# Kernel tuning notes

Measured on AMD Instinct MI355X. Metric: run time of the kernel, lower is better.

## Reference

```python
import jax, jax.numpy as jnp
import numpy as np

TEMPERATURE = 1.0  # forward default
INIT_STD = 0.01    # per-class gate init: N(0, 0.01)

def setup_inputs() -> dict:
    key = jax.random.key(0)
    kf, kws, kw1, kw2 = jax.random.split(key, 4)
    B, F, H, C, E = 256, 2048, 512, 512, 8
    Hh = H // 2  # 256
    features = jax.random.normal(kf, (B, F), dtype=jnp.float32)
    # shared transform Linear(F, H) -- default torch init approximated by small normal
    Ws = jax.random.normal(kws, (F, H), dtype=jnp.float32) * (1.0 / np.sqrt(F))
    bs = jnp.zeros((H,), dtype=jnp.float32)
    # per-class gates, stacked over class dim: N(0, 0.01) init, zero bias (as in module)
    W1 = jax.random.normal(kw1, (C, H, Hh), dtype=jnp.float32) * INIT_STD
    b1 = jnp.zeros((C, Hh), dtype=jnp.float32)
    W2 = jax.random.normal(kw2, (C, Hh, E), dtype=jnp.float32) * INIT_STD
    b2 = jnp.zeros((C, E), dtype=jnp.float32)
    return {"features": features, "Ws": Ws, "bs": bs, "W1": W1, "b1": b1, "W2": W2, "b2": b2}

def reference(features, Ws, bs, W1, b1, W2, b2):
    # shared transform: Linear -> ReLU (Dropout is identity at inference)
    shared = jax.nn.relu(features @ Ws + bs)                      # [B, H]
    # batched per-class MLP: one grouped GEMM across all classes
    h = jax.nn.relu(jnp.einsum('bh,chk->bck', shared, W1) + b1)   # [B, C, H/2]
    gate_logits = jnp.einsum('bck,cke->bce', h, W2) + b2          # [B, C, E]
    gate_weights = jax.nn.softmax(gate_logits / TEMPERATURE, axis=-1)
    return (gate_weights, gate_logits)
```

## Files before the change

### kernel.cpp

```cpp
#include <hip/hip_runtime.h>
#include <hip/hip_bf16.h>

#define BATCH 256
#define F_DIM 2048
#define H_DIM 512
#define HH    256
#define NCLS  512
#define E_DIM 8

typedef __attribute__((ext_vector_type(8))) short  bf16x8;
typedef __attribute__((ext_vector_type(4))) float  f32x4;
typedef __attribute__((ext_vector_type(4))) unsigned short u16x4;

__device__ __forceinline__ unsigned short f2bf(float x) {
    union { float f; unsigned int u; } v; v.f = x;
    unsigned int r = v.u + 0x7fffu + ((v.u >> 16) & 1u);
    return (unsigned short)(r >> 16);
}

__global__ __launch_bounds__(256) void k_gemm1(
    const float* __restrict__ features,
    const float* __restrict__ Ws,
    float* __restrict__ partials)
{
    const int tid = threadIdx.x;
    const int lane = tid & 63;
    const int wave = tid >> 6;
    const int job = blockIdx.x * 4 + wave;
    const int kidx = job & 7;
    const int ng  = (job >> 3) & 7;
    const int mt  = job >> 6;
    const int l15 = lane & 15, quad = lane >> 4;
    const int m0 = mt * 16, n0 = ng * 64, kb = kidx * 256;

    f32x4 z = {0.f, 0.f, 0.f, 0.f};
    f32x4 acc[4];
#pragma unroll
    for (int nf = 0; nf < 4; ++nf) acc[nf] = z;

#pragma unroll
    for (int ks = 0; ks < 8; ++ks) {
        const int kk = kb + ks * 32 + quad * 8;
        f32x4 a0 = *(const f32x4*)(features + (size_t)(m0 + l15) * F_DIM + kk);
        f32x4 a1 = *(const f32x4*)(features + (size_t)(m0 + l15) * F_DIM + kk + 4);
        bf16x8 aF;
#pragma unroll
        for (int j = 0; j < 4; ++j) { aF[j] = (short)f2bf(a0[j]); aF[4 + j] = (short)f2bf(a1[j]); }
#pragma unroll
        for (int nf = 0; nf < 4; ++nf) {
            bf16x8 bF;
#pragma unroll
            for (int j = 0; j < 8; ++j)
                bF[j] = (short)f2bf(Ws[(size_t)(kk + j) * H_DIM + n0 + nf * 16 + l15]);
            acc[nf] = __builtin_amdgcn_mfma_f32_16x16x32_bf16(aF, bF, acc[nf], 0, 0, 0);
        }
    }
    float* po = partials + (size_t)kidx * (BATCH * H_DIM);
#pragma unroll
    for (int nf = 0; nf < 4; ++nf)
#pragma unroll
        for (int r = 0; r < 4; ++r)
            po[(size_t)(m0 + quad * 4 + r) * H_DIM + n0 + nf * 16 + l15] = acc[nf][r];
}

__global__ __launch_bounds__(256) void k_reduce_relu(
    const float* __restrict__ partials, const float* __restrict__ bs,
    unsigned short* __restrict__ sharedA)
{
    const int idx = (blockIdx.x * 256 + threadIdx.x) * 4;
    f32x4 s = *(const f32x4*)(partials + idx);
#pragma unroll
    for (int p = 1; p < 8; ++p)
        s += *(const f32x4*)(partials + (size_t)p * (BATCH * H_DIM) + idx);
    s += *(const f32x4*)(bs + (idx & (H_DIM - 1)));
    u16x4 o;
#pragma unroll
    for (int j = 0; j < 4; ++j) {
        float v = s[j] > 0.f ? s[j] : 0.f;
        o[j] = f2bf(v);
    }
    *(u16x4*)(sharedA + idx) = o;
}

__global__ __launch_bounds__(256, 3) void k_main(
    const unsigned short* __restrict__ sharedA,
    const float* __restrict__ W1,
    const float* __restrict__ b1,
    const float* __restrict__ W2,
    float* __restrict__ part4)
{
    const int c = blockIdx.x >> 2;
    const int q = blockIdx.x & 3;
    const int tid = threadIdx.x;
    const int lane = tid & 63;
    const int wave = tid >> 6;
    const int l15 = lane & 15;
    const int quad = lane >> 4;
    const int m0w = wave * 64;
    const int colL = tid & 63;
    const int kseg = tid >> 6;

    const float* __restrict__ W1cq = W1 + (size_t)c * (H_DIM * HH) + q * 64;

    __shared__ unsigned short buf[2][8 * 64 * 8];

    f32x4 z = {0.f, 0.f, 0.f, 0.f};
    f32x4 acc[4][4];
#pragma unroll
    for (int mf = 0; mf < 4; ++mf)
#pragma unroll
        for (int nf = 0; nf < 4; ++nf) acc[mf][nf] = z;

    float rg[16];
#pragma unroll
    for (int j = 0; j < 16; ++j)
        rg[j] = W1cq[(size_t)(kseg * 16 + j) * HH + colL];

#pragma unroll
    for (int ch = 0; ch < 8; ++ch) {
        unsigned short* bp = &buf[ch & 1][0];
#pragma unroll
        for (int h = 0; h < 2; ++h) {
            bf16x8 v;
#pragma unroll
            for (int j = 0; j < 8; ++j) v[j] = (short)f2bf(rg[h * 8 + j]);
            const int kg = kseg * 2 + h;
            *(bf16x8*)(bp + ((kg * 64 + colL) << 3)) = v;
        }
        __syncthreads();
        if (ch < 7) {
#pragma unroll
            for (int j = 0; j < 16; ++j)
                rg[j] = W1cq[(size_t)((ch + 1) * 64 + kseg * 16 + j) * HH + colL];
        }
#pragma unroll
        for (int ks = 0; ks < 2; ++ks) {
            const int k0 = ch * 64 + ks * 32 + quad * 8;
            bf16x8 aF[4];
#pragma unroll
            for (int mf = 0; mf < 4; ++mf)
                aF[mf] = *(const bf16x8*)(sharedA + (size_t)(m0w + mf * 16 + l15) * H_DIM + k0);
#pragma unroll
            for (int nf = 0; nf < 4; ++nf) {
                bf16x8 bF = *(const bf16x8*)(bp + (((ks * 4 + quad) * 64 + nf * 16 + l15) << 3));
#pragma unroll
                for (int mf = 0; mf < 4; ++mf)
                    acc[mf][nf] = __builtin_amdgcn_mfma_f32_16x16x32_bf16(aF[mf], bF, acc[mf][nf], 0, 0, 0);
            }
        }
    }

    const int cq = q * 64;
    float b1v[4];
    f32x4 w2a[4], w2b[4];
#pragma unroll
    for (int nf = 0; nf < 4; ++nf) {
        const int col = cq + nf * 16 + l15;
        b1v[nf] = b1[(size_t)c * HH + col];
        w2a[nf] = *(const f32x4*)(W2 + ((size_t)c * HH + col) * E_DIM);
        w2b[nf] = *(const f32x4*)(W2 + ((size_t)c * HH + col) * E_DIM + 4);
    }

#pragma unroll
    for (int mf = 0; mf < 4; ++mf) {
        float part[4][E_DIM];
#pragma unroll
        for (int r = 0; r < 4; ++r)
#pragma unroll
            for (int e = 0; e < E_DIM; ++e) part[r][e] = 0.f;
#pragma unroll
        for (int nf = 0; nf < 4; ++nf) {
#pragma unroll
            for (int r = 0; r < 4; ++r) {
                float h = acc[mf][nf][r] + b1v[nf];
                h = h > 0.f ? h : 0.f;
                part[r][0] += h * w2a[nf][0]; part[r][1] += h * w2a[nf][1];
                part[r][2] += h * w2a[nf][2]; part[r][3] += h * w2a[nf][3];
                part[r][4] += h * w2b[nf][0]; part[r][5] += h * w2b[nf][1];
                part[r][6] += h * w2b[nf][2]; part[r][7] += h * w2b[nf][3];
            }
        }
#pragma unroll
        for (int r = 0; r < 4; ++r)
#pragma unroll
            for (int e = 0; e < E_DIM; ++e) {
                float v = part[r][e];
                v += __shfl_xor(v, 1, 16);
                v += __shfl_xor(v, 2, 16);
                v += __shfl_xor(v, 4, 16);
                v += __shfl_xor(v, 8, 16);
                part[r][e] = v;
            }
        if (l15 == 0) {
#pragma unroll
            for (int r = 0; r < 4; ++r) {
                const int row = m0w + mf * 16 + quad * 4 + r;
                f32x4 lo = {part[r][0], part[r][1], part[r][2], part[r][3]};
                f32x4 hi = {part[r][4], part[r][5], part[r][6], part[r][7]};
                float* dst = part4 + (((size_t)q * NCLS + c) * BATCH + row) * E_DIM;
                *(f32x4*)dst = lo;
                *(f32x4*)(dst + 4) = hi;
            }
        }
    }
}

__global__ __launch_bounds__(256) void k_softmax(
    const float* __restrict__ part4,
    const float* __restrict__ b2,
    float* __restrict__ out)
{
    const int c = blockIdx.x;
    const int b = threadIdx.x;

    f32x4 lg0 = {0.f, 0.f, 0.f, 0.f}, lg1 = {0.f, 0.f, 0.f, 0.f};
#pragma unroll
    for (int qq = 0; qq < 4; ++qq) {
        const float* p = part4 + (((size_t)qq * NCLS + c) * BATCH + b) * E_DIM;
        lg0 += *(const f32x4*)p;
        lg1 += *(const f32x4*)(p + 4);
    }
    lg0 += *(const f32x4*)(b2 + (size_t)c * E_DIM);
    lg1 += *(const f32x4*)(b2 + (size_t)c * E_DIM + 4);

    float lg[8] = {lg0[0], lg0[1], lg0[2], lg0[3], lg1[0], lg1[1], lg1[2], lg1[3]};
    float mx = lg[0];
#pragma unroll
    for (int e = 1; e < 8; ++e) mx = lg[e] > mx ? lg[e] : mx;
    float ex[8], s = 0.f;
#pragma unroll
    for (int e = 0; e < 8; ++e) { ex[e] = __expf(lg[e] - mx); s += ex[e]; }
    const float inv = 1.f / s;

    const size_t ob = ((size_t)b * NCLS + c) * E_DIM;
    f32x4 w0 = {ex[0] * inv, ex[1] * inv, ex[2] * inv, ex[3] * inv};
    f32x4 w1 = {ex[4] * inv, ex[5] * inv, ex[6] * inv, ex[7] * inv};
    *(f32x4*)(out + ob) = w0;
    *(f32x4*)(out + ob + 4) = w1;
    const size_t lbase = (size_t)BATCH * NCLS * E_DIM;
    f32x4 o0 = {lg[0], lg[1], lg[2], lg[3]};
    f32x4 o1 = {lg[4], lg[5], lg[6], lg[7]};
    *(f32x4*)(out + lbase + ob) = o0;
    *(f32x4*)(out + lbase + ob + 4) = o1;
}

extern "C" void kernel_launch(void* const* d_in, const int* in_sizes, int n_in,
                              void* d_out, int out_size, void* d_ws, size_t ws_size,
                              hipStream_t stream) {
    const float* features = (const float*)d_in[0];
    const float* Ws       = (const float*)d_in[1];
    const float* bs       = (const float*)d_in[2];
    const float* W1       = (const float*)d_in[3];
    const float* b1       = (const float*)d_in[4];
    const float* W2       = (const float*)d_in[5];
    const float* b2       = (const float*)d_in[6];
    float* out = (float*)d_out;

    char* ws = (char*)d_ws;
    float*          parts   = (float*)ws;
    float*          part4   = (float*)ws;
    unsigned short* sharedA = (unsigned short*)(ws + 16777216);

    hipLaunchKernelGGL(k_gemm1,       dim3(256),  dim3(256), 0, stream, features, Ws, parts);
    hipLaunchKernelGGL(k_reduce_relu, dim3(128),  dim3(256), 0, stream, parts, bs, sharedA);
    hipLaunchKernelGGL(k_main,        dim3(2048), dim3(256), 0, stream, sharedA, W1, b1, W2, part4);
    hipLaunchKernelGGL(k_softmax,     dim3(NCLS), dim3(256), 0, stream, part4, b2, out);
}
```

Measured before the change: 454.9 us.

## Load W1 fragments directly into registers, dropping LDS staging and barriers

The main kernel no longer stages W1 through a double-buffered shared-memory tile with __syncthreads. Each wave now loads its own B fragments straight from global memory into registers, two k-steps ahead, converting to bf16 just before the MFMA. The A fragments are prefetched the same way. This removes LDS traffic and barriers, but all four waves now load the same W1 columns redundantly, register pressure goes up (occupancy hint lowered from 3 to 2), and the global loads are narrow scalar strided accesses.

```diff
diff --git a/kernel.cpp b/kernel.cpp
--- a/kernel.cpp
+++ b/kernel.cpp
@@ -82,7 +82,7 @@
     *(u16x4*)(sharedA + idx) = o;
 }
 
-__global__ __launch_bounds__(256, 3) void k_main(
+__global__ __launch_bounds__(256, 2) void k_main(
     const unsigned short* __restrict__ sharedA,
     const float* __restrict__ W1,
     const float* __restrict__ b1,
@@ -97,12 +97,9 @@
     const int l15 = lane & 15;
     const int quad = lane >> 4;
     const int m0w = wave * 64;
-    const int colL = tid & 63;
-    const int kseg = tid >> 6;
-
-    const float* __restrict__ W1cq = W1 + (size_t)c * (H_DIM * HH) + q * 64;
-
-    __shared__ unsigned short buf[2][8 * 64 * 8];
+    const int n0 = q * 64;
+
+    const float* __restrict__ W1cq = W1 + (size_t)c * (H_DIM * HH) + n0;
 
     f32x4 z = {0.f, 0.f, 0.f, 0.f};
     f32x4 acc[4][4];
@@ -111,51 +108,55 @@
 #pragma unroll
         for (int nf = 0; nf < 4; ++nf) acc[mf][nf] = z;
 
-    float rg[16];
-#pragma unroll
-    for (int j = 0; j < 16; ++j)
-        rg[j] = W1cq[(size_t)(kseg * 16 + j) * HH + colL];
-
-#pragma unroll
-    for (int ch = 0; ch < 8; ++ch) {
-        unsigned short* bp = &buf[ch & 1][0];
-#pragma unroll
-        for (int h = 0; h < 2; ++h) {
-            bf16x8 v;
-#pragma unroll
-            for (int j = 0; j < 8; ++j) v[j] = (short)f2bf(rg[h * 8 + j]);
-            const int kg = kseg * 2 + h;
-            *(bf16x8*)(bp + ((kg * 64 + colL) << 3)) = v;
-        }
-        __syncthreads();
-        if (ch < 7) {
-#pragma unroll
-            for (int j = 0; j < 16; ++j)
-                rg[j] = W1cq[(size_t)((ch + 1) * 64 + kseg * 16 + j) * HH + colL];
-        }
-#pragma unroll
-        for (int ks = 0; ks < 2; ++ks) {
-            const int k0 = ch * 64 + ks * 32 + quad * 8;
-            bf16x8 aF[4];
+    float  braw[2][32];
+    bf16x8 aS[2][4];
+
+#pragma unroll
+    for (int s = 0; s < 2; ++s) {
+#pragma unroll
+        for (int nf = 0; nf < 4; ++nf)
+#pragma unroll
+            for (int jj = 0; jj < 8; ++jj)
+                braw[s][nf * 8 + jj] =
+                    W1cq[(size_t)(s * 32 + quad * 8 + jj) * HH + nf * 16 + l15];
+#pragma unroll
+        for (int mf = 0; mf < 4; ++mf)
+            aS[s][mf] = *(const bf16x8*)(sharedA + (size_t)(m0w + mf * 16 + l15) * H_DIM + s * 32 + quad * 8);
+    }
+
+#pragma unroll
+    for (int ks = 0; ks < 16; ++ks) {
+        const int cur = ks & 1;
+        bf16x8 bF[4];
+#pragma unroll
+        for (int nf = 0; nf < 4; ++nf)
+#pragma unroll
+            for (int jj = 0; jj < 8; ++jj)
+                bF[nf][jj] = (short)f2bf(braw[cur][nf * 8 + jj]);
+#pragma unroll
+        for (int nf = 0; nf < 4; ++nf)
 #pragma unroll
             for (int mf = 0; mf < 4; ++mf)
-                aF[mf] = *(const bf16x8*)(sharedA + (size_t)(m0w + mf * 16 + l15) * H_DIM + k0);
-#pragma unroll
-            for (int nf = 0; nf < 4; ++nf) {
-                bf16x8 bF = *(const bf16x8*)(bp + (((ks * 4 + quad) * 64 + nf * 16 + l15) << 3));
-#pragma unroll
-                for (int mf = 0; mf < 4; ++mf)
-                    acc[mf][nf] = __builtin_amdgcn_mfma_f32_16x16x32_bf16(aF[mf], bF, acc[mf][nf], 0, 0, 0);
-            }
-        }
-    }
-
-    const int cq = q * 64;
+                acc[mf][nf] = __builtin_amdgcn_mfma_f32_16x16x32_bf16(aS[cur][mf], bF[nf], acc[mf][nf], 0, 0, 0);
+        if (ks + 2 < 16) {
+            const int kb = (ks + 2) * 32;
+#pragma unroll
+            for (int nf = 0; nf < 4; ++nf)
+#pragma unroll
+                for (int jj = 0; jj < 8; ++jj)
+                    braw[cur][nf * 8 + jj] =
+                        W1cq[(size_t)(kb + quad * 8 + jj) * HH + nf * 16 + l15];
+#pragma unroll
+            for (int mf = 0; mf < 4; ++mf)
+                aS[cur][mf] = *(const bf16x8*)(sharedA + (size_t)(m0w + mf * 16 + l15) * H_DIM + kb + quad * 8);
+        }
+    }
+
     float b1v[4];
     f32x4 w2a[4], w2b[4];
 #pragma unroll
     for (int nf = 0; nf < 4; ++nf) {
-        const int col = cq + nf * 16 + l15;
+        const int col = n0 + nf * 16 + l15;
         b1v[nf] = b1[(size_t)c * HH + col];
         w2a[nf] = *(const f32x4*)(W2 + ((size_t)c * HH + col) * E_DIM);
         w2b[nf] = *(const f32x4*)(W2 + ((size_t)c * HH + col) * E_DIM + 4);
```

New measurement: 499.0 us. +9.7%, slower.
